# Optimization experiments

Measured on AMD Instinct MI355X. Metric: run time of the kernel, lower is better.

The kernel has to match this reference:

```python
import jax, jax.numpy as jnp
import numpy as np
import math

B, L, C_IN = 64, 3168, 64
D_MODEL, K = 512, 16  # K = cycle_length (kernel width == stride)
W = L // K            # 198 output tokens from deform conv


def _positional(S, d, dtype):
    # PositionalEmbedding buffer, rows [0, S)
    pos = jnp.arange(S, dtype=jnp.float32)[:, None]
    div = jnp.exp(jnp.arange(0, d, 2, dtype=jnp.float32) * (-math.log(10000.0) / d))
    pe = jnp.zeros((S, d), jnp.float32)
    pe = pe.at[:, 0::2].set(jnp.sin(pos * div))
    pe = pe.at[:, 1::2].set(jnp.cos(pos * div))
    return pe.astype(dtype)


def setup_inputs() -> dict:
    key = jax.random.key(0)
    ks = jax.random.split(key, 6)
    fan_in = C_IN * K
    std = math.sqrt(2.0 / (1 + 0.01 ** 2) / fan_in)  # kaiming_normal, leaky_relu fan_in
    return {
        "x": jax.random.normal(ks[0], (B, L, C_IN), jnp.float32),
        "w_off": jax.random.normal(ks[1], (2 * K, C_IN, K), jnp.float32) * std,
        "b_off": jax.random.normal(ks[2], (2 * K,), jnp.float32) * 0.02,
        "w_def": jax.random.normal(ks[3], (D_MODEL, C_IN, K), jnp.float32) * std,
        "b_def": jax.random.normal(ks[4], (D_MODEL,), jnp.float32) * 0.02,
        "cls_token": jax.random.normal(ks[5], (1, 1, D_MODEL), jnp.float32),
    }


def _gather_cols(xt, idx, L_):
    # xt: (B, C, L); idx: (B, K, W) int32 -> (B, C, K, W), zero out-of-bounds
    b, c = xt.shape[0], xt.shape[1]
    valid = (idx >= 0) & (idx < L_)
    idxc = jnp.clip(idx, 0, L_ - 1).reshape(b, 1, -1)
    g = jnp.take_along_axis(xt, jnp.broadcast_to(idxc, (b, c, idxc.shape[-1])), axis=2)
    g = g.reshape(b, c, idx.shape[1], idx.shape[2])
    return jnp.where(valid[:, None], g, 0.0)


def reference(x, w_off, b_off, w_def, b_def, cls_token):
    b, l, c = x.shape
    w = l // K
    # offset conv: kernel (1,K), stride (1,K) == non-overlapping windows
    xr = x[:, : w * K, :].reshape(b, w, K, c)              # (B, W, K, C)
    off = jnp.einsum('bwkc,ock->bow', xr, w_off) + b_off[None, :, None]  # (B, 2K, W)
    dy = off[:, 0::2]                                      # (B, K, W)
    dx = off[:, 1::2]
    # sampling positions along width (height is size 1, base y = 0)
    base = (jnp.arange(w)[None, :] * K + jnp.arange(K)[:, None]).astype(x.dtype)  # (K, W)
    px = base[None] + dx                                   # (B, K, W)
    x0 = jnp.floor(px)
    frac = px - x0
    x0i = x0.astype(jnp.int32)
    xt = x.transpose(0, 2, 1)                              # (B, C, L)
    v0 = _gather_cols(xt, x0i, l)
    v1 = _gather_cols(xt, x0i + 1, l)
    wy = jnp.maximum(0.0, 1.0 - jnp.abs(dy))               # vertical bilinear weight on row 0
    val = wy[:, None] * ((1.0 - frac)[:, None] * v0 + frac[:, None] * v1)  # (B, C, K, W)
    out = jnp.einsum('bckw,dck->bwd', val, w_def) + b_def  # (B, W, d_model)
    tok = jnp.concatenate([jnp.broadcast_to(cls_token, (b, 1, D_MODEL)), out], axis=1)
    pe = _positional(w + 1, D_MODEL, tok.dtype)
    return tok + pe[None]
```

## Files before the change

kernel.cpp:

```cpp
#include <hip/hip_runtime.h>
#include <math.h>
#include <stdint.h>

#define NB 64
#define NL 3168
#define NC 64
#define ND 512
#define NK 16
#define NW 198
#define NM 12672
#define KD 1024

typedef __attribute__((ext_vector_type(8))) short bf8_t;
typedef __attribute__((ext_vector_type(4))) float f4_t;

typedef const unsigned int __attribute__((address_space(1)))* as1_u32p;
typedef unsigned int __attribute__((address_space(3)))* as3_u32p;

__device__ __forceinline__ void gl_lds16(const void* g, void* l) {
  __builtin_amdgcn_global_load_lds((as1_u32p)(uintptr_t)g,
                                   (as3_u32p)(unsigned int)(uintptr_t)l, 16, 0, 0);
}

__device__ __forceinline__ unsigned short f2bf(float f) {
  union { float f; unsigned u; } v; v.f = f;
  unsigned r = v.u + 0x7FFFu + ((v.u >> 16) & 1u);
  return (unsigned short)(r >> 16);
}

__global__ void prep_kernel(const float* __restrict__ w_off, const float* __restrict__ w_def,
                            const float* __restrict__ cls, unsigned short* __restrict__ wofft,
                            unsigned short* __restrict__ wdeft, float* __restrict__ pe,
                            float* __restrict__ out) {
  int id = blockIdx.x * 256 + threadIdx.x;
  if (id < 524288) {
    wdeft[id] = f2bf(w_def[id]);
    return;
  }
  id -= 524288;
  if (id < 32768) {
    int o = id >> 10, kc = id & 1023, k = kc >> 6, c = kc & 63;
    wofft[id] = f2bf(w_off[o * 1024 + c * 16 + k]);
    return;
  }
  id -= 32768;
  if (id < 101888) {
    int pos = id >> 9, d = id & 511;
    int i = d >> 1;
    float freq = expf((float)(2 * i) * (-9.210340371976184f / 512.0f));
    float arg = (float)pos * freq;
    pe[id] = (d & 1) ? cosf(arg) : sinf(arg);
    return;
  }
  id -= 101888;
  {
    int b = id >> 9, d = id & 511;
    out[(size_t)(b * 199) * 512 + d] = cls[d] + ((d & 1) ? 1.0f : 0.0f);
  }
}

__launch_bounds__(256)
__global__ void offsample_kernel(const float* __restrict__ x,
                                 const unsigned short* __restrict__ wofft,
                                 const float* __restrict__ b_off,
                                 unsigned short* __restrict__ val_ws) {
  __shared__ float partial[4][16][33];
  __shared__ float offs[16][32];
  int tid = threadIdx.x;
  int lane = tid & 63, wid = tid >> 6;
  int r16 = lane & 15, kg = lane >> 4;
  int row0 = blockIdx.x * 16;

  f4_t acc[2] = {};
  const float* arow = x + (size_t)(row0 + r16) * KD + wid * 256;
  const unsigned short* bcol0 = wofft + r16 * KD + wid * 256;
  const unsigned short* bcol1 = wofft + (16 + r16) * KD + wid * 256;

#pragma unroll
  for (int ks = 0; ks < 8; ++ks) {
    int k0 = ks * 32 + kg * 8;
    float4 v0 = *(const float4*)(arow + k0);
    float4 v1 = *(const float4*)(arow + k0 + 4);
    bf8_t a;
    a[0] = (short)f2bf(v0.x); a[1] = (short)f2bf(v0.y);
    a[2] = (short)f2bf(v0.z); a[3] = (short)f2bf(v0.w);
    a[4] = (short)f2bf(v1.x); a[5] = (short)f2bf(v1.y);
    a[6] = (short)f2bf(v1.z); a[7] = (short)f2bf(v1.w);
    bf8_t b0 = *(const bf8_t*)(bcol0 + k0);
    bf8_t b1 = *(const bf8_t*)(bcol1 + k0);
    acc[0] = __builtin_amdgcn_mfma_f32_16x16x32_bf16(a, b0, acc[0], 0, 0, 0);
    acc[1] = __builtin_amdgcn_mfma_f32_16x16x32_bf16(a, b1, acc[1], 0, 0, 0);
  }
#pragma unroll
  for (int n = 0; n < 2; ++n)
#pragma unroll
    for (int r = 0; r < 4; ++r)
      partial[wid][kg * 4 + r][n * 16 + r16] = acc[n][r];
  __syncthreads();
#pragma unroll
  for (int i = 0; i < 2; ++i) {
    int idx = tid * 2 + i;
    int r = idx >> 5, o = idx & 31;
    offs[r][o] = partial[0][r][o] + partial[1][r][o] + partial[2][r][o] + partial[3][r][o]
                 + b_off[o];
  }
  __syncthreads();

#pragma unroll
  for (int rr = 0; rr < 4; ++rr) {
    int rp = wid * 4 + rr;
    int rg = row0 + rp;
    int b = rg / NW, w = rg - b * NW;
    const float* xb = x + (size_t)b * (NL * NC);
    unsigned short vv[16];
#pragma unroll
    for (int k = 0; k < 16; ++k) {
      float dy = offs[rp][2 * k], dx = offs[rp][2 * k + 1];
      float wy = fmaxf(0.f, 1.f - fabsf(dy));
      float px = (float)(w * 16 + k) + dx;
      float x0f = floorf(px);
      float frac = px - x0f;
      int x0 = (int)x0f;
      float v0 = (x0 >= 0 && x0 < NL) ? xb[x0 * 64 + lane] : 0.f;
      float v1 = (x0 + 1 >= 0 && x0 + 1 < NL) ? xb[(x0 + 1) * 64 + lane] : 0.f;
      vv[k] = f2bf(wy * ((1.f - frac) * v0 + frac * v1));
    }
    unsigned int p[8];
#pragma unroll
    for (int i = 0; i < 8; ++i)
      p[i] = (unsigned int)vv[2 * i] | ((unsigned int)vv[2 * i + 1] << 16);
    uint4* dst = (uint4*)(val_ws + (size_t)rg * KD + lane * 16);
    dst[0] = make_uint4(p[0], p[1], p[2], p[3]);
    dst[1] = make_uint4(p[4], p[5], p[6], p[7]);
  }
}

__launch_bounds__(256)
__global__ void gemm_kernel(const unsigned short* __restrict__ val_ws,
                            const unsigned short* __restrict__ wdeft,
                            const float* __restrict__ b_def, const float* __restrict__ pe,
                            float* __restrict__ out) {
  __shared__ unsigned short As[2][128 * 64];
  __shared__ unsigned short Bs[2][128 * 64];
  int tid = threadIdx.x;
  int mt = blockIdx.x, nt = blockIdx.y;
  int lane = tid & 63, wid = tid >> 6;
  int r16 = lane & 15, kg = lane >> 4;
  int wr = wid >> 1, wc = wid & 1;
  f4_t acc[4][4] = {};

  int r_st = lane >> 3;
  int j_st = lane & 7;
  const char* aBase = (const char*)val_ws + (size_t)mt * 128 * 2048;
  const char* bBase = (const char*)wdeft + (size_t)nt * 128 * 2048;

  auto STAGE = [&](int ks, int buf) {
#pragma unroll
    for (int i = 0; i < 4; ++i) {
      int seg = wid * 4 + i;
      int r = seg * 8 + r_st;
      int src_off = ((j_st ^ (r & 7)) << 4);
      gl_lds16(aBase + (size_t)r * 2048 + ks * 128 + src_off, &As[buf][seg * 512]);
      gl_lds16(bBase + (size_t)r * 2048 + ks * 128 + src_off, &Bs[buf][seg * 512]);
    }
  };

  auto COMPUTE = [&](int buf) {
#pragma unroll
    for (int jb = 0; jb < 8; jb += 4) {
      bf8_t af[4], bf[4];
#pragma unroll
      for (int m = 0; m < 4; ++m) {
        int R = wr * 64 + m * 16 + r16;
        af[m] = *(const bf8_t*)&As[buf][R * 64 + (((jb + kg) ^ (R & 7)) << 3)];
      }
#pragma unroll
      for (int n = 0; n < 4; ++n) {
        int Rc = wc * 64 + n * 16 + r16;
        bf[n] = *(const bf8_t*)&Bs[buf][Rc * 64 + (((jb + kg) ^ (Rc & 7)) << 3)];
      }
#pragma unroll
      for (int m = 0; m < 4; ++m)
#pragma unroll
        for (int n = 0; n < 4; ++n)
          acc[m][n] = __builtin_amdgcn_mfma_f32_16x16x32_bf16(af[m], bf[n], acc[m][n], 0, 0, 0);
    }
  };

  STAGE(0, 0);
  __syncthreads();
#pragma unroll
  for (int ks = 0; ks < 15; ++ks) {
    STAGE(ks + 1, (ks + 1) & 1);
    COMPUTE(ks & 1);
    __syncthreads();
  }
  COMPUTE(1);

#pragma unroll
  for (int m = 0; m < 4; ++m)
#pragma unroll
    for (int n = 0; n < 4; ++n)
#pragma unroll
      for (int r = 0; r < 4; ++r) {
        int grow = mt * 128 + wr * 64 + m * 16 + kg * 4 + r;
        int gcol = nt * 128 + wc * 64 + n * 16 + r16;
        int bi = grow / NW, wi = grow - bi * NW;
        out[((size_t)(bi * 199 + wi + 1)) * 512 + gcol] =
            acc[m][n][r] + b_def[gcol] + pe[(wi + 1) * 512 + gcol];
      }
}

extern "C" void kernel_launch(void* const* d_in, const int* in_sizes, int n_in,
                              void* d_out, int out_size, void* d_ws, size_t ws_size,
                              hipStream_t stream) {
  const float* x     = (const float*)d_in[0];
  const float* w_off = (const float*)d_in[1];
  const float* b_off = (const float*)d_in[2];
  const float* w_def = (const float*)d_in[3];
  const float* b_def = (const float*)d_in[4];
  const float* cls   = (const float*)d_in[5];
  float* out = (float*)d_out;
  char* ws = (char*)d_ws;
  unsigned short* val_ws = (unsigned short*)ws;
  unsigned short* wofft  = (unsigned short*)(ws + 25952256);
  unsigned short* wdeft  = (unsigned short*)(ws + 26017792);
  float* pe              = (float*)(ws + 27066368);

  prep_kernel<<<2702, 256, 0, stream>>>(w_off, w_def, cls, wofft, wdeft, pe, out);
  offsample_kernel<<<NM / 16, 256, 0, stream>>>(x, wofft, b_off, val_ws);
  gemm_kernel<<<dim3(99, 4), 256, 0, stream>>>(val_ws, wdeft, b_def, pe, out);
}
```

Before: 70.09 us.

## Split offset GEMM from sampling, shrink GEMM N-tile, vectorize weight prep

The fused offset-conv plus sampling kernel is split in two. The offset GEMM now writes offsets to a workspace, and a separate sample kernel runs one wave per output row with a much larger grid to raise parallelism for the gather. The main GEMM tile narrows from 128x128 to 128x64, giving 792 blocks instead of 396, with a remapped block order so neighbouring blocks share A tiles in cache. The w_def bf16 conversion is vectorised to float4. The split adds a kernel launch and an offset round-trip through global memory, and the smaller N-tile lowers MFMA reuse per block.

```diff
diff --git a/kernel.cpp b/kernel.cpp
--- a/kernel.cpp
+++ b/kernel.cpp
@@ -33,11 +33,14 @@
                             unsigned short* __restrict__ wdeft, float* __restrict__ pe,
                             float* __restrict__ out) {
   int id = blockIdx.x * 256 + threadIdx.x;
-  if (id < 524288) {
-    wdeft[id] = f2bf(w_def[id]);
+  if (id < 131072) {
+    float4 v = ((const float4*)w_def)[id];
+    ushort4 o;
+    o.x = f2bf(v.x); o.y = f2bf(v.y); o.z = f2bf(v.z); o.w = f2bf(v.w);
+    ((ushort4*)wdeft)[id] = o;
     return;
   }
-  id -= 524288;
+  id -= 131072;
   if (id < 32768) {
     int o = id >> 10, kc = id & 1023, k = kc >> 6, c = kc & 63;
     wofft[id] = f2bf(w_off[o * 1024 + c * 16 + k]);
@@ -60,12 +63,9 @@
 }
 
 __launch_bounds__(256)
-__global__ void offsample_kernel(const float* __restrict__ x,
-                                 const unsigned short* __restrict__ wofft,
-                                 const float* __restrict__ b_off,
-                                 unsigned short* __restrict__ val_ws) {
+__global__ void offgemm_kernel(const float* __restrict__ x, const unsigned short* __restrict__ wofft,
+                               const float* __restrict__ b_off, float* __restrict__ off_ws) {
   __shared__ float partial[4][16][33];
-  __shared__ float offs[16][32];
   int tid = threadIdx.x;
   int lane = tid & 63, wid = tid >> 6;
   int r16 = lane & 15, kg = lane >> 4;
@@ -101,38 +101,39 @@
   for (int i = 0; i < 2; ++i) {
     int idx = tid * 2 + i;
     int r = idx >> 5, o = idx & 31;
-    offs[r][o] = partial[0][r][o] + partial[1][r][o] + partial[2][r][o] + partial[3][r][o]
-                 + b_off[o];
-  }
-  __syncthreads();
-
-#pragma unroll
-  for (int rr = 0; rr < 4; ++rr) {
-    int rp = wid * 4 + rr;
-    int rg = row0 + rp;
-    int b = rg / NW, w = rg - b * NW;
-    const float* xb = x + (size_t)b * (NL * NC);
-    unsigned short vv[16];
-#pragma unroll
-    for (int k = 0; k < 16; ++k) {
-      float dy = offs[rp][2 * k], dx = offs[rp][2 * k + 1];
-      float wy = fmaxf(0.f, 1.f - fabsf(dy));
-      float px = (float)(w * 16 + k) + dx;
-      float x0f = floorf(px);
-      float frac = px - x0f;
-      int x0 = (int)x0f;
-      float v0 = (x0 >= 0 && x0 < NL) ? xb[x0 * 64 + lane] : 0.f;
-      float v1 = (x0 + 1 >= 0 && x0 + 1 < NL) ? xb[(x0 + 1) * 64 + lane] : 0.f;
-      vv[k] = f2bf(wy * ((1.f - frac) * v0 + frac * v1));
-    }
-    unsigned int p[8];
-#pragma unroll
-    for (int i = 0; i < 8; ++i)
-      p[i] = (unsigned int)vv[2 * i] | ((unsigned int)vv[2 * i + 1] << 16);
-    uint4* dst = (uint4*)(val_ws + (size_t)rg * KD + lane * 16);
-    dst[0] = make_uint4(p[0], p[1], p[2], p[3]);
-    dst[1] = make_uint4(p[4], p[5], p[6], p[7]);
-  }
+    float s = partial[0][r][o] + partial[1][r][o] + partial[2][r][o] + partial[3][r][o];
+    off_ws[(row0 + r) * 32 + o] = s + b_off[o];
+  }
+}
+
+__global__ void sample_kernel(const float* __restrict__ x, const float* __restrict__ off_ws,
+                              unsigned short* __restrict__ val_ws) {
+  int tid = threadIdx.x;
+  int wid = tid >> 6, lane = tid & 63;
+  int row = blockIdx.x * 4 + wid;
+  int b = row / NW, w = row - b * NW;
+  const float* xb = x + (size_t)b * (NL * NC);
+  const float* offr = off_ws + row * 32;
+  unsigned short vv[16];
+#pragma unroll
+  for (int k = 0; k < 16; ++k) {
+    float dy = offr[2 * k], dx = offr[2 * k + 1];
+    float wy = fmaxf(0.f, 1.f - fabsf(dy));
+    float px = (float)(w * 16 + k) + dx;
+    float x0f = floorf(px);
+    float frac = px - x0f;
+    int x0 = (int)x0f;
+    float v0 = (x0 >= 0 && x0 < NL) ? xb[x0 * 64 + lane] : 0.f;
+    float v1 = (x0 + 1 >= 0 && x0 + 1 < NL) ? xb[(x0 + 1) * 64 + lane] : 0.f;
+    vv[k] = f2bf(wy * ((1.f - frac) * v0 + frac * v1));
+  }
+  unsigned int p[8];
+#pragma unroll
+  for (int i = 0; i < 8; ++i)
+    p[i] = (unsigned int)vv[2 * i] | ((unsigned int)vv[2 * i + 1] << 16);
+  uint4* dst = (uint4*)(val_ws + (size_t)row * KD + lane * 16);
+  dst[0] = make_uint4(p[0], p[1], p[2], p[3]);
+  dst[1] = make_uint4(p[4], p[5], p[6], p[7]);
 }
 
 __launch_bounds__(256)
@@ -141,18 +142,20 @@
                             const float* __restrict__ b_def, const float* __restrict__ pe,
                             float* __restrict__ out) {
   __shared__ unsigned short As[2][128 * 64];
-  __shared__ unsigned short Bs[2][128 * 64];
+  __shared__ unsigned short Bs[2][64 * 64];
   int tid = threadIdx.x;
-  int mt = blockIdx.x, nt = blockIdx.y;
+  int flat = blockIdx.x + 8 * blockIdx.y;
+  int wk = (flat & 7) * 99 + (flat >> 3);
+  int nt = wk & 7, mt = wk >> 3;
   int lane = tid & 63, wid = tid >> 6;
   int r16 = lane & 15, kg = lane >> 4;
   int wr = wid >> 1, wc = wid & 1;
-  f4_t acc[4][4] = {};
+  f4_t acc[4][2] = {};
 
   int r_st = lane >> 3;
   int j_st = lane & 7;
   const char* aBase = (const char*)val_ws + (size_t)mt * 128 * 2048;
-  const char* bBase = (const char*)wdeft + (size_t)nt * 128 * 2048;
+  const char* bBase = (const char*)wdeft + (size_t)nt * 64 * 2048;
 
   auto STAGE = [&](int ks, int buf) {
 #pragma unroll
@@ -161,6 +164,12 @@
       int r = seg * 8 + r_st;
       int src_off = ((j_st ^ (r & 7)) << 4);
       gl_lds16(aBase + (size_t)r * 2048 + ks * 128 + src_off, &As[buf][seg * 512]);
+    }
+#pragma unroll
+    for (int i = 0; i < 2; ++i) {
+      int seg = wid * 2 + i;
+      int r = seg * 8 + r_st;
+      int src_off = ((j_st ^ (r & 7)) << 4);
       gl_lds16(bBase + (size_t)r * 2048 + ks * 128 + src_off, &Bs[buf][seg * 512]);
     }
   };
@@ -168,22 +177,22 @@
   auto COMPUTE = [&](int buf) {
 #pragma unroll
     for (int jb = 0; jb < 8; jb += 4) {
-      bf8_t af[4], bf[4];
+      bf8_t af[4], bf2[2];
 #pragma unroll
       for (int m = 0; m < 4; ++m) {
         int R = wr * 64 + m * 16 + r16;
         af[m] = *(const bf8_t*)&As[buf][R * 64 + (((jb + kg) ^ (R & 7)) << 3)];
       }
 #pragma unroll
-      for (int n = 0; n < 4; ++n) {
-        int Rc = wc * 64 + n * 16 + r16;
-        bf[n] = *(const bf8_t*)&Bs[buf][Rc * 64 + (((jb + kg) ^ (Rc & 7)) << 3)];
+      for (int n = 0; n < 2; ++n) {
+        int Rc = wc * 32 + n * 16 + r16;
+        bf2[n] = *(const bf8_t*)&Bs[buf][Rc * 64 + (((jb + kg) ^ (Rc & 7)) << 3)];
       }
 #pragma unroll
       for (int m = 0; m < 4; ++m)
 #pragma unroll
-        for (int n = 0; n < 4; ++n)
-          acc[m][n] = __builtin_amdgcn_mfma_f32_16x16x32_bf16(af[m], bf[n], acc[m][n], 0, 0, 0);
+        for (int n = 0; n < 2; ++n)
+          acc[m][n] = __builtin_amdgcn_mfma_f32_16x16x32_bf16(af[m], bf2[n], acc[m][n], 0, 0, 0);
     }
   };
 
@@ -200,11 +209,11 @@
 #pragma unroll
   for (int m = 0; m < 4; ++m)
 #pragma unroll
-    for (int n = 0; n < 4; ++n)
+    for (int n = 0; n < 2; ++n)
 #pragma unroll
       for (int r = 0; r < 4; ++r) {
         int grow = mt * 128 + wr * 64 + m * 16 + kg * 4 + r;
-        int gcol = nt * 128 + wc * 64 + n * 16 + r16;
+        int gcol = nt * 64 + wc * 32 + n * 16 + r16;
         int bi = grow / NW, wi = grow - bi * NW;
         out[((size_t)(bi * 199 + wi + 1)) * 512 + gcol] =
             acc[m][n][r] + b_def[gcol] + pe[(wi + 1) * 512 + gcol];
@@ -226,8 +235,10 @@
   unsigned short* wofft  = (unsigned short*)(ws + 25952256);
   unsigned short* wdeft  = (unsigned short*)(ws + 26017792);
   float* pe              = (float*)(ws + 27066368);
-
-  prep_kernel<<<2702, 256, 0, stream>>>(w_off, w_def, cls, wofft, wdeft, pe, out);
-  offsample_kernel<<<NM / 16, 256, 0, stream>>>(x, wofft, b_off, val_ws);
-  gemm_kernel<<<dim3(99, 4), 256, 0, stream>>>(val_ws, wdeft, b_def, pe, out);
-}
+  float* off_ws          = (float*)(ws + 27473920);
+
+  prep_kernel<<<1166, 256, 0, stream>>>(w_off, w_def, cls, wofft, wdeft, pe, out);
+  offgemm_kernel<<<NM / 16, 256, 0, stream>>>(x, wofft, b_off, off_ws);
+  sample_kernel<<<NM / 4, 256, 0, stream>>>(x, off_ws, val_ws);
+  gemm_kernel<<<dim3(8, 99), 256, 0, stream>>>(val_ws, wdeft, b_def, pe, out);
+}
```

After: 78.82 us. +12.4%, slower.
